# Performance work log

Hardware: AMD Instinct MI355X
Metric: run time of the kernel (lower is better)

Reference implementation:

```python
import jax, jax.numpy as jnp
import numpy as np
from jax import lax

ALPHA = float(np.exp(-1.0 / 5.0))   # exp(-1/tau_mem), tau_mem=5.0
THRESHOLD = 1.0


def _dwconv(x, w, b, groups):
    # x: (B, Cin, T), w: (Cout, Cin/groups, K), 'same' padding for odd K
    pad = (w.shape[-1] - 1) // 2
    y = lax.conv_general_dilated(
        x, w, window_strides=(1,), padding=[(pad, pad)],
        dimension_numbers=("NCH", "OIH", "NCH"), feature_group_count=groups)
    return y + b[None, :, None]


def setup_inputs() -> dict:
    key = jax.random.key(0)
    ks = jax.random.split(key, 12)
    B, C, T = 8, 256, 4096
    OP = 6            # out_per_kernel for each of the 3 kernel sizes
    DEC = 128         # decoder_channels
    f32 = jnp.float32
    d = {}
    d["x"] = jax.random.normal(ks[0], (B, C, T), f32)
    # depthwise multi-path conv params (groups=C): weight (C*OP, 1, K)
    d["w3"] = jax.random.normal(ks[1], (C * OP, 1, 3), f32) * 0.2
    d["b3"] = jnp.zeros((C * OP,), f32)
    d["w5"] = jax.random.normal(ks[2], (C * OP, 1, 5), f32) * 0.15
    d["b5"] = jnp.zeros((C * OP,), f32)
    d["w9"] = jax.random.normal(ks[3], (C * OP, 1, 9), f32) * 0.1
    d["b9"] = jnp.zeros((C * OP,), f32)
    # reduce: Conv1d(C*18 -> C, k=1, groups=C): weight (C, 18, 1)
    d["w_red"] = jax.random.normal(ks[4], (C, 3 * OP, 1), f32) * 0.2
    d["b_red"] = jnp.zeros((C,), f32)
    d["latency_scale"] = jnp.asarray(5.0, f32)
    # output_gates: xavier uniform (C, C) with zero diagonal
    bound = float(np.sqrt(6.0 / (C + C)))
    og = jax.random.uniform(ks[5], (C, C), f32, -bound, bound)
    d["output_gates"] = og * (1.0 - jnp.eye(C, dtype=f32))
    d["bias"] = jnp.zeros((C,), f32)
    # post_mlp: Linear(C, DEC) -> ReLU -> Linear(DEC, C); stored as (in, out)
    d["W1"] = jax.random.normal(ks[6], (C, DEC), f32) * float(np.sqrt(2.0 / C))
    d["b1"] = jnp.zeros((DEC,), f32)
    d["W2"] = jax.random.normal(ks[7], (DEC, C), f32) * float(np.sqrt(2.0 / DEC))
    d["b2"] = jnp.zeros((C,), f32)
    return d


def reference(x, w3, b3, w5, b5, w9, b9, w_red, b_red,
              latency_scale, output_gates, bias, W1, b1, W2, b2):
    B, C, T = x.shape
    # DepthwiseMultiPathEncoder: 3 depthwise convs -> cat -> grouped 1x1 reduce
    o3 = _dwconv(x, w3, b3, C)
    o5 = _dwconv(x, w5, b5, C)
    o9 = _dwconv(x, w9, b9, C)
    cat = jnp.concatenate([o3, o5, o9], axis=1)      # (B, 18C, T)
    drive = _dwconv(cat, w_red, b_red, C)             # (B, C, T)
    # LIF membrane recurrence + first-spike latency (sequential over T)
    d_t = jnp.moveaxis(drive, 2, 0)                   # (T, B, C)
    def step(V, dt):
        V = ALPHA * V + (1.0 - ALPHA) * dt
        return V, V >= THRESHOLD
    _, crossed = lax.scan(step, jnp.zeros((B, C), x.dtype), d_t)  # (T, B, C) bool
    fired_any = crossed.any(axis=0)
    first_t = jnp.argmax(crossed, axis=0)             # first True index
    true_latency = jnp.where(fired_any, first_t, T).astype(x.dtype)  # (B, C)
    # latency -> activation -> gated mix -> MLP -> softplus, clamp [0, T]
    scale = jnp.maximum(latency_scale, 0.001)
    act = jnp.exp(-true_latency / scale)              # (B, C)
    mixed = act @ output_gates.T + bias[None, :]      # (B, C)
    h = jax.nn.relu(mixed @ W1 + b1)
    raw_pred = h @ W2 + b2
    pred_latency = jnp.clip(jax.nn.softplus(raw_pred), 0.0, float(T))
    return pred_latency, true_latency, act
```

## Files before the change

kernel.cpp:

```cpp
#include <hip/hip_runtime.h>
#include <math.h>

#define C_CH 256
#define T_LEN 4096


#define LOAD_ROW(xa, r) do {                                                  \
    const int src_ = (jj + (r)) & 255;                                        \
    const float4* p_ = (const float4*)(x + ((size_t)b * C_CH + src_) * T_LEN + t0); \
    float4 qm_ = tid ? p_[-1] : p_[0];                                        \
    float4 q0_ = p_[0], q1_ = p_[1];                                          \
    float4 q2_ = (tid < 511) ? p_[2] : p_[1];                                 \
    if (tid == 0)   qm_ = make_float4(0.f, 0.f, 0.f, 0.f);                    \
    if (tid == 511) q2_ = make_float4(0.f, 0.f, 0.f, 0.f);                    \
    xa[0]  = qm_.x; xa[1]  = qm_.y; xa[2]  = qm_.z; xa[3]  = qm_.w;           \
    xa[4]  = q0_.x; xa[5]  = q0_.y; xa[6]  = q0_.z; xa[7]  = q0_.w;           \
    xa[8]  = q1_.x; xa[9]  = q1_.y; xa[10] = q1_.z; xa[11] = q1_.w;           \
    xa[12] = q2_.x; xa[13] = q2_.y; xa[14] = q2_.z; xa[15] = q2_.w;           \
} while (0)

__global__ __launch_bounds__(512, 4) void drive_scan_kernel(
    const float* __restrict__ x,
    const float* __restrict__ w3, const float* __restrict__ b3,
    const float* __restrict__ w5, const float* __restrict__ b5,
    const float* __restrict__ w9, const float* __restrict__ b9,
    const float* __restrict__ w_red, const float* __restrict__ b_red,
    const float* __restrict__ latency_scale,
    const float* __restrict__ og, const float* __restrict__ W1,
    const float* __restrict__ W2, float* __restrict__ ogT,
    float* __restrict__ sink,
    float* __restrict__ out_lat, float* __restrict__ out_act)
{
    const int blk = blockIdx.x;
    const int tid = threadIdx.x;

    if (blk < 8) {
        const int id = blk * 512 + tid;
        const float4* og4 = (const float4*)og;
        const float4* W14 = (const float4*)W1;
        const float4* W24 = (const float4*)W2;
        const int jrow  = id >> 4;
        const int ibase = (id & 15) << 4;
        #pragma unroll
        for (int v = 0; v < 4; ++v) {
            float4 q = og4[id * 4 + v];
            const int i = ibase + v * 4;
            ogT[(i + 0) * 256 + jrow] = q.x;
            ogT[(i + 1) * 256 + jrow] = q.y;
            ogT[(i + 2) * 256 + jrow] = q.z;
            ogT[(i + 3) * 256 + jrow] = q.w;
        }
        float acc = 0.0f;
        #pragma unroll
        for (int v = 0; v < 2; ++v) {
            float4 q = W14[id + v * 4096]; acc += q.x + q.y + q.z + q.w;
        }
        #pragma unroll
        for (int v = 0; v < 2; ++v) {
            float4 q = W24[id + v * 4096]; acc += q.x + q.y + q.z + q.w;
        }
        sink[id] = acc;
        return;
    }

    const int bb   = blk - 8;
    const int b    = bb >> 8;
    const int i255 = bb & 255;
    const int jj   = ((i255 & 7) << 5) | (i255 >> 3);
    const int c    = (171 * jj) & 255;
    const int lane = tid & 63;
    const int wv   = tid >> 6;

    __shared__ float sWaveTot[8];
    __shared__ float sCarry[8];
    __shared__ int   sMin[8];

    const int t0 = tid << 3;

    float foldv = 0.0f;
    if (lane < 27) {
        const int r = lane / 9, k = lane - 9 * r;
        const int q0     = 18 * c + 6 * r;
        const int region = (q0 >= 1536) + (q0 >= 3072);
        const int p0     = q0 - region * 1536;
        const int K      = (region == 0) ? 3 : (region == 1 ? 5 : 9);
        const int off    = (9 - K) >> 1;
        const float* wP  = (region == 0) ? w3 : (region == 1 ? w5 : w9);
        const int kk     = k - off;
        if (kk >= 0 && kk < K) {
            const float* wr = w_red + c * 18 + 6 * r;
            #pragma unroll
            for (int j = 0; j < 6; ++j)
                foldv = fmaf(wr[j], wP[(p0 + j) * K + kk], foldv);
        }
    } else if (lane == 27) {
        float acc = b_red[c];
        #pragma unroll
        for (int r = 0; r < 3; ++r) {
            const int q0     = 18 * c + 6 * r;
            const int region = (q0 >= 1536) + (q0 >= 3072);
            const int p0     = q0 - region * 1536;
            const float* bP  = (region == 0) ? b3 : (region == 1 ? b5 : b9);
            const float* wr  = w_red + c * 18 + 6 * r;
            #pragma unroll
            for (int j = 0; j < 6; ++j) acc = fmaf(wr[j], bP[p0 + j], acc);
        }
        foldv = acc;
    }

    float xa0[16], xa1[16], xa2[16];
    LOAD_ROW(xa0, 0);
    LOAD_ROW(xa1, 1);
    LOAD_ROW(xa2, 2);

    float d[8];
    {
        const float Beff = __shfl(foldv, 27, 64);
        #pragma unroll
        for (int tt = 0; tt < 8; ++tt) d[tt] = Beff;
    }
    #pragma unroll
    for (int k = 0; k < 9; ++k) {
        const float wk = __shfl(foldv, k, 64);
        #pragma unroll
        for (int tt = 0; tt < 8; ++tt)
            d[tt] = fmaf(wk, xa0[tt + k], d[tt]);
    }
    #pragma unroll
    for (int k = 0; k < 9; ++k) {
        const float wk = __shfl(foldv, 9 + k, 64);
        #pragma unroll
        for (int tt = 0; tt < 8; ++tt)
            d[tt] = fmaf(wk, xa1[tt + k], d[tt]);
    }
    #pragma unroll
    for (int k = 0; k < 9; ++k) {
        const float wk = __shfl(foldv, 18 + k, 64);
        #pragma unroll
        for (int tt = 0; tt < 8; ++tt)
            d[tt] = fmaf(wk, xa2[tt + k], d[tt]);
    }

    const float A   = (float)0.8187307530779818;
    const float OMA = (float)(1.0 - 0.8187307530779818);

    float S = 0.0f;
    #pragma unroll
    for (int tt = 0; tt < 8; ++tt) S = A * S + OMA * d[tt];

    const float Fp[6] = {
        (float)2.0189651799465541e-01,
        (float)4.0762203978366215e-02,
        (float)1.6615572731739337e-03,
        (float)2.7607725720371943e-06,
        (float)7.6218649302532563e-12,
        (float)5.8092835977683129e-23
    };
    float cinc = S;
    #pragma unroll
    for (int s = 0; s < 6; ++s) {
        const int o = 1 << s;
        const float y = __shfl_up(cinc, o, 64);
        if (lane >= o) cinc = fmaf(Fp[s], y, cinc);
    }
    if (lane == 63) sWaveTot[wv] = cinc;
    __syncthreads();
    if (tid == 0) {
        const float A512 = 3.3744728758705166e-45f;
        float g = 0.0f;
        #pragma unroll
        for (int w = 0; w < 8; ++w) { sCarry[w] = g; g = sWaveTot[w] + A512 * g; }
    }
    __syncthreads();
    const float cprev = __shfl_up(cinc, 1, 64);
    const float Vin = (lane ? cprev : 0.0f)
                    + expf(-1.6f * (float)lane) * sCarry[wv];

    float V = Vin;
    int firstT = T_LEN;
    #pragma unroll
    for (int tt = 0; tt < 8; ++tt) {
        V = A * V + OMA * d[tt];
        if (V >= 1.0f && firstT == T_LEN) firstT = t0 + tt;
    }

    #pragma unroll
    for (int o = 32; o > 0; o >>= 1)
        firstT = min(firstT, __shfl_xor(firstT, o, 64));
    if (lane == 0) sMin[wv] = firstT;
    __syncthreads();
    if (tid == 0) {
        int f = sMin[0];
        #pragma unroll
        for (int w = 1; w < 8; ++w) f = min(f, sMin[w]);
        const float lat   = (float)f;
        const float scale = fmaxf(latency_scale[0], 0.001f);
        out_lat[(b << 8) + c] = lat;
        out_act[(b << 8) + c] = expf(-lat / scale);
    }
}

__global__ __launch_bounds__(512) void mlp_kernel(
    const float* __restrict__ act,
    const float* __restrict__ ogT, const float* __restrict__ bias,
    const float* __restrict__ W1, const float* __restrict__ b1,
    const float* __restrict__ W2, const float* __restrict__ b2,
    float* __restrict__ out_pred)
{
    const int b = blockIdx.x;
    const int t = threadIdx.x;
    const int j = t & 255;
    const int g = t >> 8;

    __shared__ float sAct[256];
    __shared__ float sP[2][256];
    __shared__ float sMix[256];
    __shared__ float sPH[4][128];
    __shared__ float sH[128];
    __shared__ float sPR[2][256];

    if (t < 256) sAct[t] = act[b * 256 + t];
    __syncthreads();

    float mix = 0.0f;
    {
        const float* col = ogT + (size_t)(g * 128) * 256 + j;
        const float* a   = sAct + g * 128;
        #pragma unroll 16
        for (int ii = 0; ii < 128; ++ii)
            mix = fmaf(a[ii], col[ii * 256], mix);
    }
    sP[g][j] = mix;
    __syncthreads();
    if (t < 256) sMix[t] = bias[t] + sP[0][t] + sP[1][t];
    __syncthreads();

    {
        const int j1  = t & 127;
        const int seg = t >> 7;
        float h = 0.0f;
        #pragma unroll
        for (int ii = 0; ii < 64; ++ii) {
            const int i = seg * 64 + ii;
            h = fmaf(sMix[i], W1[i * 128 + j1], h);
        }
        sPH[seg][j1] = h;
    }
    __syncthreads();
    if (t < 128)
        sH[t] = fmaxf(b1[t] + ((sPH[0][t] + sPH[1][t]) + (sPH[2][t] + sPH[3][t])), 0.0f);
    __syncthreads();

    {
        float raw = 0.0f;
        #pragma unroll
        for (int kk = 0; kk < 64; ++kk) {
            const int k = g * 64 + kk;
            raw = fmaf(sH[k], W2[k * 256 + j], raw);
        }
        sPR[g][j] = raw;
    }
    __syncthreads();
    if (t < 256) {
        const float r  = b2[t] + sPR[0][t] + sPR[1][t];
        const float sp = fmaxf(r, 0.0f) + log1pf(expf(-fabsf(r)));
        out_pred[b * 256 + t] = fminf(fmaxf(sp, 0.0f), 4096.0f);
    }
}

extern "C" void kernel_launch(void* const* d_in, const int* in_sizes, int n_in,
                              void* d_out, int out_size, void* d_ws, size_t ws_size,
                              hipStream_t stream) {
    const float* x    = (const float*)d_in[0];
    const float* w3   = (const float*)d_in[1];
    const float* b3   = (const float*)d_in[2];
    const float* w5   = (const float*)d_in[3];
    const float* b5   = (const float*)d_in[4];
    const float* w9   = (const float*)d_in[5];
    const float* b9   = (const float*)d_in[6];
    const float* wred = (const float*)d_in[7];
    const float* bred = (const float*)d_in[8];
    const float* ls   = (const float*)d_in[9];
    const float* og   = (const float*)d_in[10];
    const float* bias = (const float*)d_in[11];
    const float* W1   = (const float*)d_in[12];
    const float* b1   = (const float*)d_in[13];
    const float* W2   = (const float*)d_in[14];
    const float* b2   = (const float*)d_in[15];

    float* ogT      = (float*)d_ws;
    float* sink     = (float*)d_ws + 65536;
    float* out      = (float*)d_out;
    float* out_pred = out;
    float* out_lat  = out + 2048;
    float* out_act  = out + 4096;

    drive_scan_kernel<<<2056, 512, 0, stream>>>(
        x, w3, b3, w5, b5, w9, b9, wred, bred, ls,
        og, W1, W2, ogT, sink, out_lat, out_act);
    mlp_kernel<<<8, 512, 0, stream>>>(out_act, ogT, bias, W1, b1, W2, b2, out_pred);
}
```

Measured before the change: 123.6 us.

## Map one wave per channel with 64 timesteps per lane, drop block-level scan

Restructures the drive/scan kernel so each 64-lane wave handles a whole (batch, channel) row of 4096 timesteps, with every lane computing 64 consecutive outputs from a sliding register window of float4 loads. Block count falls from 2056 to 264, each block covering 8 channels. The cross-wave shared-memory carry and the __syncthreads barriers go away, and the in-wave scan needs only 4 shuffle steps because the decay over 64 steps is tiny. In exchange each lane holds far more registers (64 drive values plus window), occupancy drops (launch bounds lowered to 2), and fewer blocks may leave CUs idle.

```diff
diff --git a/kernel.cpp b/kernel.cpp
--- a/kernel.cpp
+++ b/kernel.cpp
@@ -5,21 +5,7 @@
 #define T_LEN 4096
 
 
-#define LOAD_ROW(xa, r) do {                                                  \
-    const int src_ = (jj + (r)) & 255;                                        \
-    const float4* p_ = (const float4*)(x + ((size_t)b * C_CH + src_) * T_LEN + t0); \
-    float4 qm_ = tid ? p_[-1] : p_[0];                                        \
-    float4 q0_ = p_[0], q1_ = p_[1];                                          \
-    float4 q2_ = (tid < 511) ? p_[2] : p_[1];                                 \
-    if (tid == 0)   qm_ = make_float4(0.f, 0.f, 0.f, 0.f);                    \
-    if (tid == 511) q2_ = make_float4(0.f, 0.f, 0.f, 0.f);                    \
-    xa[0]  = qm_.x; xa[1]  = qm_.y; xa[2]  = qm_.z; xa[3]  = qm_.w;           \
-    xa[4]  = q0_.x; xa[5]  = q0_.y; xa[6]  = q0_.z; xa[7]  = q0_.w;           \
-    xa[8]  = q1_.x; xa[9]  = q1_.y; xa[10] = q1_.z; xa[11] = q1_.w;           \
-    xa[12] = q2_.x; xa[13] = q2_.y; xa[14] = q2_.z; xa[15] = q2_.w;           \
-} while (0)
-
-__global__ __launch_bounds__(512, 4) void drive_scan_kernel(
+__global__ __launch_bounds__(512, 2) void drive_scan_kernel(
     const float* __restrict__ x,
     const float* __restrict__ w3, const float* __restrict__ b3,
     const float* __restrict__ w5, const float* __restrict__ b5,
@@ -63,19 +49,14 @@
         return;
     }
 
-    const int bb   = blk - 8;
-    const int b    = bb >> 8;
-    const int i255 = bb & 255;
-    const int jj   = ((i255 & 7) << 5) | (i255 >> 3);
-    const int c    = (171 * jj) & 255;
-    const int lane = tid & 63;
-    const int wv   = tid >> 6;
-
-    __shared__ float sWaveTot[8];
-    __shared__ float sCarry[8];
-    __shared__ int   sMin[8];
-
-    const int t0 = tid << 3;
+    const int bb     = blk - 8;
+    const int b      = bb >> 5;
+    const int i31    = bb & 31;
+    const int jjband = ((i31 & 7) << 2) | (i31 >> 3);
+    const int lane   = tid & 63;
+    const int wv     = tid >> 6;
+    const int jj     = (jjband << 3) | wv;
+    const int c      = (171 * jj) & 255;
 
     float foldv = 0.0f;
     if (lane < 27) {
@@ -108,37 +89,72 @@
         foldv = acc;
     }
 
-    float xa0[16], xa1[16], xa2[16];
-    LOAD_ROW(xa0, 0);
-    LOAD_ROW(xa1, 1);
-    LOAD_ROW(xa2, 2);
-
-    float d[8];
-    {
-        const float Beff = __shfl(foldv, 27, 64);
-        #pragma unroll
-        for (int tt = 0; tt < 8; ++tt) d[tt] = Beff;
-    }
-    #pragma unroll
-    for (int k = 0; k < 9; ++k) {
-        const float wk = __shfl(foldv, k, 64);
-        #pragma unroll
-        for (int tt = 0; tt < 8; ++tt)
-            d[tt] = fmaf(wk, xa0[tt + k], d[tt]);
-    }
-    #pragma unroll
-    for (int k = 0; k < 9; ++k) {
-        const float wk = __shfl(foldv, 9 + k, 64);
-        #pragma unroll
-        for (int tt = 0; tt < 8; ++tt)
-            d[tt] = fmaf(wk, xa1[tt + k], d[tt]);
-    }
-    #pragma unroll
-    for (int k = 0; k < 9; ++k) {
-        const float wk = __shfl(foldv, 18 + k, 64);
-        #pragma unroll
-        for (int tt = 0; tt < 8; ++tt)
-            d[tt] = fmaf(wk, xa2[tt + k], d[tt]);
+    float tap[27];
+    #pragma unroll
+    for (int k = 0; k < 27; ++k) tap[k] = __shfl(foldv, k, 64);
+    const float Beff = __shfl(foldv, 27, 64);
+
+    const float4 Z4 = make_float4(0.f, 0.f, 0.f, 0.f);
+    const float4* P0 = (const float4*)(x + ((size_t)b * C_CH + ((jj    ) & 255)) * T_LEN) + (lane * 16 - 1);
+    const float4* P1 = (const float4*)(x + ((size_t)b * C_CH + ((jj + 1) & 255)) * T_LEN) + (lane * 16 - 1);
+    const float4* P2 = (const float4*)(x + ((size_t)b * C_CH + ((jj + 2) & 255)) * T_LEN) + (lane * 16 - 1);
+
+    const int m0 = lane ? 0 : 1;
+    float4 aP = P0[m0], bP = P1[m0], cP = P2[m0];
+    if (lane == 0) { aP = Z4; bP = Z4; cP = Z4; }
+    float4 aQ0 = P0[1], aQ1 = P0[2], aN = P0[3];
+    float4 bQ0 = P1[1], bQ1 = P1[2], bN = P1[3];
+    float4 cQ0 = P2[1], cQ1 = P2[2], cN = P2[3];
+
+    float d[64];
+
+    #pragma unroll
+    for (int cc = 0; cc < 8; ++cc) {
+        float4 aX, aY, bX, bY, cX, cY;
+        if (cc < 7) {
+            const int m4 = 2 * cc + 4;
+            aX = P0[m4]; bX = P1[m4]; cX = P2[m4];
+            const int m5 = (cc == 6) ? ((lane == 63) ? 16 : 17) : (2 * cc + 5);
+            aY = P0[m5]; bY = P1[m5]; cY = P2[m5];
+            if (cc == 6 && lane == 63) { aY = Z4; bY = Z4; cY = Z4; }
+        }
+
+        const float w0[16] = { aP.x, aP.y, aP.z, aP.w, aQ0.x, aQ0.y, aQ0.z, aQ0.w,
+                               aQ1.x, aQ1.y, aQ1.z, aQ1.w, aN.x, aN.y, aN.z, aN.w };
+        const float w1[16] = { bP.x, bP.y, bP.z, bP.w, bQ0.x, bQ0.y, bQ0.z, bQ0.w,
+                               bQ1.x, bQ1.y, bQ1.z, bQ1.w, bN.x, bN.y, bN.z, bN.w };
+        const float w2[16] = { cP.x, cP.y, cP.z, cP.w, cQ0.x, cQ0.y, cQ0.z, cQ0.w,
+                               cQ1.x, cQ1.y, cQ1.z, cQ1.w, cN.x, cN.y, cN.z, cN.w };
+
+        #pragma unroll
+        for (int tt = 0; tt < 8; ++tt) d[cc * 8 + tt] = Beff;
+        #pragma unroll
+        for (int k = 0; k < 9; ++k) {
+            const float wk = tap[k];
+            #pragma unroll
+            for (int tt = 0; tt < 8; ++tt)
+                d[cc * 8 + tt] = fmaf(wk, w0[tt + k], d[cc * 8 + tt]);
+        }
+        #pragma unroll
+        for (int k = 0; k < 9; ++k) {
+            const float wk = tap[9 + k];
+            #pragma unroll
+            for (int tt = 0; tt < 8; ++tt)
+                d[cc * 8 + tt] = fmaf(wk, w1[tt + k], d[cc * 8 + tt]);
+        }
+        #pragma unroll
+        for (int k = 0; k < 9; ++k) {
+            const float wk = tap[18 + k];
+            #pragma unroll
+            for (int tt = 0; tt < 8; ++tt)
+                d[cc * 8 + tt] = fmaf(wk, w2[tt + k], d[cc * 8 + tt]);
+        }
+
+        if (cc < 7) {
+            aP = aQ1; aQ0 = aN; aQ1 = aX; aN = aY;
+            bP = bQ1; bQ0 = bN; bQ1 = bX; bN = bY;
+            cP = cQ1; cQ0 = cN; cQ1 = cX; cN = cY;
+        }
     }
 
     const float A   = (float)0.8187307530779818;
@@ -146,54 +162,38 @@
 
     float S = 0.0f;
     #pragma unroll
-    for (int tt = 0; tt < 8; ++tt) S = A * S + OMA * d[tt];
-
-    const float Fp[6] = {
-        (float)2.0189651799465541e-01,
-        (float)4.0762203978366215e-02,
-        (float)1.6615572731739337e-03,
+    for (int t = 0; t < 64; ++t) S = A * S + OMA * d[t];
+
+    const float Fp[4] = {
         (float)2.7607725720371943e-06,
         (float)7.6218649302532563e-12,
-        (float)5.8092835977683129e-23
+        (float)5.8092835977683129e-23,
+        (float)3.3744728758705166e-45
     };
     float cinc = S;
     #pragma unroll
-    for (int s = 0; s < 6; ++s) {
+    for (int s = 0; s < 4; ++s) {
         const int o = 1 << s;
         const float y = __shfl_up(cinc, o, 64);
         if (lane >= o) cinc = fmaf(Fp[s], y, cinc);
     }
-    if (lane == 63) sWaveTot[wv] = cinc;
-    __syncthreads();
-    if (tid == 0) {
-        const float A512 = 3.3744728758705166e-45f;
-        float g = 0.0f;
-        #pragma unroll
-        for (int w = 0; w < 8; ++w) { sCarry[w] = g; g = sWaveTot[w] + A512 * g; }
-    }
-    __syncthreads();
     const float cprev = __shfl_up(cinc, 1, 64);
-    const float Vin = (lane ? cprev : 0.0f)
-                    + expf(-1.6f * (float)lane) * sCarry[wv];
+    const float Vin = lane ? cprev : 0.0f;
 
     float V = Vin;
     int firstT = T_LEN;
-    #pragma unroll
-    for (int tt = 0; tt < 8; ++tt) {
-        V = A * V + OMA * d[tt];
-        if (V >= 1.0f && firstT == T_LEN) firstT = t0 + tt;
+    const int tb = lane << 6;
+    #pragma unroll
+    for (int t = 0; t < 64; ++t) {
+        V = A * V + OMA * d[t];
+        if (V >= 1.0f && firstT == T_LEN) firstT = tb + t;
     }
 
     #pragma unroll
     for (int o = 32; o > 0; o >>= 1)
         firstT = min(firstT, __shfl_xor(firstT, o, 64));
-    if (lane == 0) sMin[wv] = firstT;
-    __syncthreads();
-    if (tid == 0) {
-        int f = sMin[0];
-        #pragma unroll
-        for (int w = 1; w < 8; ++w) f = min(f, sMin[w]);
-        const float lat   = (float)f;
+    if (lane == 0) {
+        const float lat   = (float)firstT;
         const float scale = fmaxf(latency_scale[0], 0.001f);
         out_lat[(b << 8) + c] = lat;
         out_act[(b << 8) + c] = expf(-lat / scale);
@@ -295,7 +295,7 @@
     float* out_lat  = out + 2048;
     float* out_act  = out + 4096;
 
-    drive_scan_kernel<<<2056, 512, 0, stream>>>(
+    drive_scan_kernel<<<264, 512, 0, stream>>>(
         x, w3, b3, w5, b5, w9, b9, wred, bred, ls,
         og, W1, W2, ogT, sink, out_lat, out_act);
     mlp_kernel<<<8, 512, 0, stream>>>(out_act, ogT, bias, W1, b1, W2, b2, out_pred);
```

Result: slower. 131.3 us (+6.2%).
